# Kernel optimization log

Hardware: AMD Instinct MI355X
Metric: run time of the kernel (lower is better)

Reference implementation:

```python
import jax, jax.numpy as jnp
import numpy as np

IGNORE = -100000.0

def setup_inputs() -> dict:
    key = jax.random.key(0)
    ks = jax.random.split(key, 5)
    B, S, E, H, D = 4, 2048, 1024, 16, 64
    return {
        "x": jax.random.normal(ks[0], (B, S, E), dtype=jnp.float32),
        "W_Q": jax.random.normal(ks[1], (H, E, D), dtype=jnp.float32) * (E ** -0.5),
        "W_K": jax.random.normal(ks[2], (H, E, D), dtype=jnp.float32) * (E ** -0.5),
        "W_V": jax.random.normal(ks[3], (H, E, D), dtype=jnp.float32) * (E ** -0.5),
        "W_O": jax.random.normal(ks[4], (H, D, E), dtype=jnp.float32) * (D ** -0.5),
        "is_causal": 1,
    }

def reference(x, W_Q, W_K, W_V, W_O, is_causal):
    d_head = W_Q.shape[-1]
    # projections: [b, p, n_heads, d_head]
    q = jnp.einsum('nmd,bpm->bpnd', W_Q, x)
    k = jnp.einsum('nmd,bpm->bpnd', W_K, x)
    v = jnp.einsum('nmd,bpm->bpnd', W_V, x)
    # scores: [b, n_heads, q_pos, k_pos]
    scores = jnp.einsum('bqnd,bknd->bnqk', q, k) / np.sqrt(d_head).astype(jnp.float32)
    if is_causal:
        S = scores.shape[-1]
        mask = jnp.triu(jnp.ones((S, S), dtype=bool), k=1)  # True above diagonal
        scores = jnp.where(mask, jnp.float32(IGNORE), scores)
    attn = jax.nn.softmax(scores, axis=-1)
    # weighted values: [b, q_pos, n_heads, d_head]
    z = jnp.einsum('bknd,bnqk->bqnd', v, attn)
    # output projection: [b, q_pos, embed_dim]
    o = jnp.einsum('ndm,bqnd->bqm', W_O, z)
    # average_attn_weights=True -> mean over heads
    return o, attn.mean(axis=1)
```

## Files before the change

### kernel.cpp

```cpp
#include <hip/hip_runtime.h>
#include <stdint.h>


#define BB 4
#define SS 2048
#define EE 1024
#define HH 16
#define DD 64
#define MTOT (BB*SS)
#define HD (HH*DD)
#define QKV_ELEMS ((size_t)MTOT*HD)

typedef float f32x4 __attribute__((ext_vector_type(4)));
typedef short bf16x8 __attribute__((ext_vector_type(8)));

#define GLL(g, l) __builtin_amdgcn_global_load_lds( \
    (const __attribute__((address_space(1))) void*)(g), \
    (__attribute__((address_space(3))) void*)(l), 16, 0, 0)

__device__ __forceinline__ short f2bf(float f) {
    unsigned u = __builtin_bit_cast(unsigned, f);
    u += 0x7FFFu + ((u >> 16) & 1u);
    return (short)(u >> 16);
}

__global__ __launch_bounds__(256) void k_xcast(const float* __restrict__ x,
                                               short* __restrict__ xbf) {
    int i = blockIdx.x*256 + threadIdx.x;
    float4 f = ((const float4*)x)[i];
    short4 s; s.x=f2bf(f.x); s.y=f2bf(f.y); s.z=f2bf(f.z); s.w=f2bf(f.w);
    ((short4*)xbf)[i] = s;
}

__global__ __launch_bounds__(256) void k_wprep(const float* __restrict__ wq,
        const float* __restrict__ wk, const float* __restrict__ wv,
        const float* __restrict__ wo, short* __restrict__ wtq,
        short* __restrict__ wto) {
    __shared__ short Tl[64][72];
    int t = threadIdx.x, x = blockIdx.x, y = blockIdx.y;
    int r4 = t >> 2, c4 = (t & 3) << 4;
    if (y < 48) {
        int which = y >> 4, h = y & 15, e0 = x*64;
        const float* src = (which==0?wq:which==1?wk:wv) + (size_t)h*EE*DD;
        const float* p = src + (size_t)(e0 + r4)*DD + c4;
        #pragma unroll
        for (int j = 0; j < 4; ++j) {
            float4 f = ((const float4*)p)[j];
            Tl[r4][c4+j*4+0]=f2bf(f.x); Tl[r4][c4+j*4+1]=f2bf(f.y);
            Tl[r4][c4+j*4+2]=f2bf(f.z); Tl[r4][c4+j*4+3]=f2bf(f.w);
        }
        __syncthreads();
        size_t nrow = ((size_t)(which*16 + h))*64 + r4;
        #pragma unroll
        for (int i = 0; i < 16; ++i)
            wtq[nrow*1024 + e0 + c4 + i] = Tl[c4+i][r4];
    } else {
        int h = y - 48, e0 = x*64;
        const float* src = wo + (size_t)h*DD*EE;
        const float* p = src + (size_t)r4*EE + e0 + c4;
        #pragma unroll
        for (int j = 0; j < 4; ++j) {
            float4 f = ((const float4*)p)[j];
            Tl[r4][c4+j*4+0]=f2bf(f.x); Tl[r4][c4+j*4+1]=f2bf(f.y);
            Tl[r4][c4+j*4+2]=f2bf(f.z); Tl[r4][c4+j*4+3]=f2bf(f.w);
        }
        __syncthreads();
        #pragma unroll
        for (int i = 0; i < 16; ++i)
            wto[(size_t)(e0 + r4)*1024 + h*64 + c4 + i] = Tl[c4+i][r4];
    }
}

__global__ __launch_bounds__(256) void k_proj(const short* __restrict__ xbf,
        const short* __restrict__ wtq, short* __restrict__ qkv) {
    __shared__ short As[128*64];
    __shared__ short Bs[128*64];
    int t = threadIdx.x;
    int m0 = blockIdx.x*128, n0 = blockIdx.y*128;
    int lane = t & 63, l15 = lane & 15, quad = lane >> 4;
    int wm = (t>>6) >> 1, wn = (t>>6) & 1;
    f32x4 acc[4][4];
    #pragma unroll
    for (int i=0;i<4;++i)
        #pragma unroll
        for (int c=0;c<4;++c) acc[i][c] = (f32x4){0,0,0,0};

    for (int k0 = 0; k0 < EE; k0 += 64) {
        __syncthreads();
        #pragma unroll
        for (int j = 0; j < 4; ++j) {
            int c = j*256 + t;
            int row = c >> 3, cg = c & 7;
            GLL(xbf + (size_t)(m0+row)*EE + k0 + cg*8, &As[(j*256 + (t & 192))*8]);
            GLL(wtq + (size_t)(n0+row)*EE + k0 + cg*8, &Bs[(j*256 + (t & 192))*8]);
        }
        __syncthreads();
        #pragma unroll
        for (int kp = 0; kp < 64; kp += 32)
            #pragma unroll
            for (int i = 0; i < 4; ++i) {
                bf16x8 a = *(const bf16x8*)&As[(wm*64 + i*16 + l15)*64 + kp + quad*8];
                #pragma unroll
                for (int c = 0; c < 4; ++c) {
                    bf16x8 b = *(const bf16x8*)&Bs[(wn*64 + c*16 + l15)*64 + kp + quad*8];
                    acc[i][c] = __builtin_amdgcn_mfma_f32_16x16x32_bf16(a, b, acc[i][c], 0, 0, 0);
                }
            }
    }
    short* vt = qkv + 2*QKV_ELEMS;
    #pragma unroll
    for (int i = 0; i < 4; ++i)
        #pragma unroll
        for (int c = 0; c < 4; ++c) {
            int n = n0 + wn*64 + c*16 + l15;
            int row = m0 + wm*64 + i*16 + quad*4;
            if (n < 2048) {
                #pragma unroll
                for (int r = 0; r < 4; ++r)
                    qkv[(size_t)(n>>10)*QKV_ELEMS + (size_t)(row+r)*HD + (n & 1023)] =
                        f2bf(acc[i][c][r]);
            } else {
                short4 s4;
                s4.x = f2bf(acc[i][c][0]); s4.y = f2bf(acc[i][c][1]);
                s4.z = f2bf(acc[i][c][2]); s4.w = f2bf(acc[i][c][3]);
                int bb_ = row >> 11, pos = row & 2047;
                *(short4*)&vt[((size_t)bb_*HD + (n - 2048))*SS + pos] = s4;
            }
        }
}

__global__ __launch_bounds__(256) void k_attnz(const short* __restrict__ qws,
        const short* __restrict__ kws, const short* __restrict__ vtg,
        short* __restrict__ zws, float* __restrict__ c2ws) {
    __shared__ short Ks[64][72];
    __shared__ short Vt[64][72];
    __shared__ short Ps[4][32][72];
    int t = threadIdx.x;
    int h = blockIdx.y, b = blockIdx.z;
    int qx = (b & 1) ? (15 - blockIdx.x) : blockIdx.x;
    int q0 = qx*128;
    int w = t>>6, lane = t&63, l15 = lane&15, quad = lane>>4;
    int sr = t>>2, sc = (t&3)<<4;

    bf16x8 qr[2][2];
    #pragma unroll
    for (int mf=0; mf<2; ++mf)
        #pragma unroll
        for (int kp=0; kp<2; ++kp)
            qr[mf][kp] = *(const bf16x8*)(qws +
                (size_t)(b*SS + q0 + w*32 + mf*16 + l15)*HD + h*DD + kp*32 + quad*8);

    const short* ksrc = kws + (size_t)(b*SS + sr)*HD + h*DD + sc;
    const short* vsrc = vtg + ((size_t)b*HD + h*DD + sr)*SS + sc;

    f32x4 accz[2][4];
    f32x4 accl[2];
    #pragma unroll
    for (int mf=0;mf<2;++mf) {
        accl[mf] = (f32x4){0,0,0,0};
        #pragma unroll
        for (int c=0;c<4;++c) accz[mf][c] = (f32x4){0,0,0,0};
    }
    bf16x8 ones;
    #pragma unroll
    for (int i=0;i<8;++i) ones[i] = (short)0x3F80;
    const float SC = 0.125f * 1.4426950408889634f;
    int nk = q0/64 + 2;
    int qmax = q0 + w*32 + 31;

    uint4 pk0 = ((const uint4*)ksrc)[0], pk1 = ((const uint4*)ksrc)[1];
    uint4 pv0 = ((const uint4*)vsrc)[0], pv1 = ((const uint4*)vsrc)[1];

    for (int kt = 0; kt < nk; ++kt) {
        int k0 = kt*64;
        __syncthreads();
        *(uint4*)&Ks[sr][sc]   = pk0;  *(uint4*)&Ks[sr][sc+8] = pk1;
        *(uint4*)&Vt[sr][sc]   = pv0;  *(uint4*)&Vt[sr][sc+8] = pv1;
        __syncthreads();
        if (kt+1 < nk) {
            const uint4* kn = (const uint4*)(ksrc + (size_t)(k0+64)*HD);
            const uint4* vn = (const uint4*)(vsrc + (k0+64));
            pk0=kn[0]; pk1=kn[1]; pv0=vn[0]; pv1=vn[1];
        }
        if (k0 > qmax) continue;

        f32x4 s[2][4];
        #pragma unroll
        for (int mf=0;mf<2;++mf)
            #pragma unroll
            for (int c=0;c<4;++c) s[mf][c] = (f32x4){0,0,0,0};
        __builtin_amdgcn_s_setprio(1);
        #pragma unroll
        for (int c=0;c<4;++c)
            #pragma unroll
            for (int kp=0;kp<2;++kp) {
                bf16x8 bb = *(const bf16x8*)&Ks[c*16+l15][kp*32+quad*8];
                s[0][c] = __builtin_amdgcn_mfma_f32_16x16x32_bf16(qr[0][kp], bb, s[0][c], 0, 0, 0);
                s[1][c] = __builtin_amdgcn_mfma_f32_16x16x32_bf16(qr[1][kp], bb, s[1][c], 0, 0, 0);
            }
        __builtin_amdgcn_s_setprio(0);
        #pragma unroll
        for (int mf=0;mf<2;++mf) {
            int qg0 = q0 + w*32 + mf*16 + quad*4;
            #pragma unroll
            for (int c=0;c<4;++c) {
                int kg = k0 + c*16 + l15;
                #pragma unroll
                for (int r=0;r<4;++r) {
                    float p_ = (kg <= qg0+r) ? __builtin_amdgcn_exp2f(s[mf][c][r]*SC) : 0.0f;
                    Ps[w][mf*16 + quad*4 + r][c*16 + l15] = f2bf(p_);
                }
            }
        }
        __builtin_amdgcn_s_setprio(1);
        #pragma unroll
        for (int kp=0;kp<2;++kp) {
            bf16x8 pa0 = *(const bf16x8*)&Ps[w][l15][kp*32+quad*8];
            bf16x8 pa1 = *(const bf16x8*)&Ps[w][16+l15][kp*32+quad*8];
            #pragma unroll
            for (int cc=0;cc<4;++cc) {
                bf16x8 vb = *(const bf16x8*)&Vt[cc*16+l15][kp*32+quad*8];
                accz[0][cc] = __builtin_amdgcn_mfma_f32_16x16x32_bf16(pa0, vb, accz[0][cc], 0, 0, 0);
                accz[1][cc] = __builtin_amdgcn_mfma_f32_16x16x32_bf16(pa1, vb, accz[1][cc], 0, 0, 0);
            }
            accl[0] = __builtin_amdgcn_mfma_f32_16x16x32_bf16(pa0, ones, accl[0], 0, 0, 0);
            accl[1] = __builtin_amdgcn_mfma_f32_16x16x32_bf16(pa1, ones, accl[1], 0, 0, 0);
        }
        __builtin_amdgcn_s_setprio(0);
    }
    #pragma unroll
    for (int mf=0;mf<2;++mf) {
        float il[4];
        #pragma unroll
        for (int r=0;r<4;++r) il[r] = 1.0f / accl[mf][r];
        #pragma unroll
        for (int cc=0;cc<4;++cc)
            #pragma unroll
            for (int r=0;r<4;++r) {
                int row = q0 + w*32 + mf*16 + quad*4 + r;
                zws[(size_t)(b*SS+row)*HD + h*DD + cc*16 + l15] = f2bf(accz[mf][cc][r]*il[r]);
            }
        if (l15 == 0) {
            size_t base = ((size_t)(b*HH+h))*SS + q0 + w*32 + mf*16 + quad*4;
            #pragma unroll
            for (int r=0;r<4;++r)
                c2ws[base+r] = __log2f(accl[mf][r]);
        }
    }
}

__global__ __launch_bounds__(256) void k_mean(const short* __restrict__ qws,
        const short* __restrict__ kws, const float* __restrict__ c2ws,
        float* __restrict__ attn_out) {
    int b = blockIdx.z;
    int qx = (b & 1) ? (31 - (int)blockIdx.x) : (int)blockIdx.x;
    int q0 = qx*64, k0 = blockIdx.y*64;
    int t = threadIdx.x;
    if (k0 > q0) {
        int r = t >> 2, cq = (t & 3) << 4;
        float4 z4 = {0.f,0.f,0.f,0.f};
        float* dst = attn_out + ((size_t)(b*SS + q0 + r))*SS + k0 + cq;
        #pragma unroll
        for (int j = 0; j < 4; ++j) ((float4*)dst)[j] = z4;
        return;
    }
    __shared__ short Qs[2][64][72];
    __shared__ short Ks[2][64][72];
    __shared__ float c2s[16][64];
    int w = t>>6, lane = t&63, l15 = lane&15, quad = lane>>4;
    int sr = t>>2, sc = (t&3)<<4;
    #pragma unroll
    for (int i = 0; i < 4; ++i) {
        int idx = t + i*256;
        int h = idx >> 6, r = idx & 63;
        c2s[h][r] = c2ws[((size_t)(b*HH+h))*SS + q0 + r];
    }
    const short* qsrc = qws + (size_t)(b*SS + q0 + sr)*HD + sc;
    const short* ksrc = kws + (size_t)(b*SS + k0 + sr)*HD + sc;

    {
        const uint4* qp = (const uint4*)qsrc;
        const uint4* kp = (const uint4*)ksrc;
        uint4 a=qp[0], bq=qp[1], c=kp[0], d=kp[1];
        *(uint4*)&Qs[0][sr][sc]   = a;  *(uint4*)&Qs[0][sr][sc+8] = bq;
        *(uint4*)&Ks[0][sr][sc]   = c;  *(uint4*)&Ks[0][sr][sc+8] = d;
    }

    const float SC = 0.125f * 1.4426950408889634f;
    int rowg0 = q0 + w*16 + quad*4;
    f32x4 acc[4] = { {0,0,0,0},{0,0,0,0},{0,0,0,0},{0,0,0,0} };

    for (int h = 0; h < HH; ++h) {
        int cur = h & 1;
        __syncthreads();
        uint4 nqa, nqb, nka, nkb;
        if (h < HH-1) {
            const uint4* qn = (const uint4*)(qsrc + (h+1)*64);
            const uint4* kn = (const uint4*)(ksrc + (h+1)*64);
            nqa=qn[0]; nqb=qn[1]; nka=kn[0]; nkb=kn[1];
        }

        bf16x8 qa0 = *(const bf16x8*)&Qs[cur][w*16+l15][quad*8];
        bf16x8 qa1 = *(const bf16x8*)&Qs[cur][w*16+l15][quad*8+32];
        f32x4 c2 = *(const f32x4*)&c2s[h][w*16 + quad*4];
        #pragma unroll
        for (int ns = 0; ns < 4; ++ns) {
            bf16x8 b0 = *(const bf16x8*)&Ks[cur][ns*16+l15][quad*8];
            bf16x8 b1 = *(const bf16x8*)&Ks[cur][ns*16+l15][quad*8+32];
            f32x4 s = {0,0,0,0};
            s = __builtin_amdgcn_mfma_f32_16x16x32_bf16(qa0, b0, s, 0, 0, 0);
            s = __builtin_amdgcn_mfma_f32_16x16x32_bf16(qa1, b1, s, 0, 0, 0);
            int col = k0 + ns*16 + l15;
            #pragma unroll
            for (int r = 0; r < 4; ++r) {
                float ex = __builtin_amdgcn_exp2f(s[r]*SC - c2[r]);
                acc[ns][r] += (col <= rowg0 + r) ? ex : 0.0f;
            }
        }

        if (h < HH-1) {
            int nxt = cur ^ 1;
            *(uint4*)&Qs[nxt][sr][sc]   = nqa;  *(uint4*)&Qs[nxt][sr][sc+8] = nqb;
            *(uint4*)&Ks[nxt][sr][sc]   = nka;  *(uint4*)&Ks[nxt][sr][sc+8] = nkb;
        }
    }
    #pragma unroll
    for (int ns = 0; ns < 4; ++ns)
        #pragma unroll
        for (int r = 0; r < 4; ++r)
            attn_out[((size_t)(b*SS + rowg0 + r))*SS + k0 + ns*16 + l15] =
                acc[ns][r] * 0.0625f;
}

__global__ __launch_bounds__(256) void k_oproj(const short* __restrict__ zws,
        const short* __restrict__ wto, float* __restrict__ outp) {
    __shared__ short As[128*64];
    __shared__ short Bs[128*64];
    int t = threadIdx.x;
    int m0 = blockIdx.x*128, n0 = blockIdx.y*128;
    int lane = t & 63, l15 = lane & 15, quad = lane >> 4;
    int wm = (t>>6) >> 1, wn = (t>>6) & 1;
    f32x4 acc[4][4];
    #pragma unroll
    for (int i=0;i<4;++i)
        #pragma unroll
        for (int c=0;c<4;++c) acc[i][c] = (f32x4){0,0,0,0};

    for (int k0 = 0; k0 < HD; k0 += 64) {
        __syncthreads();
        #pragma unroll
        for (int j = 0; j < 4; ++j) {
            int c = j*256 + t;
            int row = c >> 3, cg = c & 7;
            GLL(zws + (size_t)(m0+row)*HD + k0 + cg*8, &As[(j*256 + (t & 192))*8]);
            GLL(wto + (size_t)(n0+row)*HD + k0 + cg*8, &Bs[(j*256 + (t & 192))*8]);
        }
        __syncthreads();
        #pragma unroll
        for (int kp = 0; kp < 64; kp += 32)
            #pragma unroll
            for (int i = 0; i < 4; ++i) {
                bf16x8 a = *(const bf16x8*)&As[(wm*64 + i*16 + l15)*64 + kp + quad*8];
                #pragma unroll
                for (int c = 0; c < 4; ++c) {
                    bf16x8 b = *(const bf16x8*)&Bs[(wn*64 + c*16 + l15)*64 + kp + quad*8];
                    acc[i][c] = __builtin_amdgcn_mfma_f32_16x16x32_bf16(a, b, acc[i][c], 0, 0, 0);
                }
            }
    }
    #pragma unroll
    for (int i = 0; i < 4; ++i)
        #pragma unroll
        for (int c = 0; c < 4; ++c)
            #pragma unroll
            for (int r = 0; r < 4; ++r) {
                int row = m0 + wm*64 + i*16 + quad*4 + r;
                int n = n0 + wn*64 + c*16 + l15;
                outp[(size_t)row*EE + n] = acc[i][c][r];
            }
}

extern "C" void kernel_launch(void* const* d_in, const int* in_sizes, int n_in,
                              void* d_out, int out_size, void* d_ws, size_t ws_size,
                              hipStream_t stream) {
    const float* x  = (const float*)d_in[0];
    const float* wq = (const float*)d_in[1];
    const float* wk = (const float*)d_in[2];
    const float* wv = (const float*)d_in[3];
    const float* wo = (const float*)d_in[4];

    short* xbf = (short*)d_ws;
    short* qb  = xbf + QKV_ELEMS;
    short* kb  = qb + QKV_ELEMS;
    short* vtb = kb + QKV_ELEMS;
    short* wtq = vtb + QKV_ELEMS;
    short* wto = wtq + (size_t)3*1024*1024;
    float* c2w = (float*)(wto + (size_t)1024*1024);
    short* zb  = xbf;

    float* o = (float*)d_out;
    float* attn_out = o + (size_t)MTOT*EE;

    k_xcast<<<dim3(8192),     256, 0, stream>>>(x, xbf);
    k_wprep<<<dim3(16,64),    256, 0, stream>>>(wq, wk, wv, wo, wtq, wto);
    k_proj <<<dim3(64,24),    256, 0, stream>>>(xbf, wtq, qb);
    k_attnz<<<dim3(16,16,4),  256, 0, stream>>>(qb, kb, vtb, zb, c2w);
    k_mean <<<dim3(32,32,4),  256, 0, stream>>>(qb, kb, c2w, attn_out);
    k_oproj<<<dim3(64,8),     256, 0, stream>>>(zb, wto, o);
}
```

Measured before the change: 391.0 us.

## Pair complementary causal query tiles per attention block and keep Q in registers

Each k_attnz block now processes two query tiles, qx and 15-qx, in one pass over the shared K/V stream. This balances causal work across blocks, halves the grid, and reuses each staged K/V tile for both. The QK^T MFMA operands are swapped so each lane holds consecutive keys, which lets P be written to LDS as short4 vectors. In k_mean, Q fragments are loaded straight from global memory into registers instead of being staged through double-buffered LDS, freeing LDS and some sync traffic at the cost of more registers.

Measured after the change: 402.0 us. +2.8%, slower.

```diff
diff --git a/kernel.cpp b/kernel.cpp
--- a/kernel.cpp
+++ b/kernel.cpp
@@ -137,39 +137,91 @@
     __shared__ short Ps[4][32][72];
     int t = threadIdx.x;
     int h = blockIdx.y, b = blockIdx.z;
-    int qx = (b & 1) ? (15 - blockIdx.x) : blockIdx.x;
-    int q0 = qx*128;
+    int bx = blockIdx.x;
+    int qxa = (b >= 2) ? (7 - bx) : bx;
+    int q0a = qxa*128, q0b = (15 - qxa)*128;
+    int nk  = 32 - 2*qxa;
     int w = t>>6, lane = t&63, l15 = lane&15, quad = lane>>4;
     int sr = t>>2, sc = (t&3)<<4;
 
-    bf16x8 qr[2][2];
-    #pragma unroll
-    for (int mf=0; mf<2; ++mf)
-        #pragma unroll
-        for (int kp=0; kp<2; ++kp)
-            qr[mf][kp] = *(const bf16x8*)(qws +
-                (size_t)(b*SS + q0 + w*32 + mf*16 + l15)*HD + h*DD + kp*32 + quad*8);
-
     const short* ksrc = kws + (size_t)(b*SS + sr)*HD + h*DD + sc;
     const short* vsrc = vtg + ((size_t)b*HD + h*DD + sr)*SS + sc;
 
-    f32x4 accz[2][4];
-    f32x4 accl[2];
+    bf16x8 qA[2][2], qB[2][2];
+    #pragma unroll
+    for (int mf=0; mf<2; ++mf)
+        #pragma unroll
+        for (int kp=0; kp<2; ++kp) {
+            qA[mf][kp] = *(const bf16x8*)(qws +
+                (size_t)(b*SS + q0a + w*32 + mf*16 + l15)*HD + h*DD + kp*32 + quad*8);
+            qB[mf][kp] = *(const bf16x8*)(qws +
+                (size_t)(b*SS + q0b + w*32 + mf*16 + l15)*HD + h*DD + kp*32 + quad*8);
+        }
+
+    f32x4 azA[2][4], azB[2][4], alA[2], alB[2];
     #pragma unroll
     for (int mf=0;mf<2;++mf) {
-        accl[mf] = (f32x4){0,0,0,0};
-        #pragma unroll
-        for (int c=0;c<4;++c) accz[mf][c] = (f32x4){0,0,0,0};
+        alA[mf] = (f32x4){0,0,0,0}; alB[mf] = (f32x4){0,0,0,0};
+        #pragma unroll
+        for (int c=0;c<4;++c) { azA[mf][c] = (f32x4){0,0,0,0}; azB[mf][c] = (f32x4){0,0,0,0}; }
     }
     bf16x8 ones;
     #pragma unroll
     for (int i=0;i<8;++i) ones[i] = (short)0x3F80;
     const float SC = 0.125f * 1.4426950408889634f;
-    int nk = q0/64 + 2;
-    int qmax = q0 + w*32 + 31;
+    int qmaxA = q0a + w*32 + 31, qmaxB = q0b + w*32 + 31;
 
     uint4 pk0 = ((const uint4*)ksrc)[0], pk1 = ((const uint4*)ksrc)[1];
     uint4 pv0 = ((const uint4*)vsrc)[0], pv1 = ((const uint4*)vsrc)[1];
+
+#define TILE(QF, AZ, AL, Q0, QMAX)                                             \
+    if (k0 <= (QMAX)) {                                                        \
+        f32x4 s_[2][4];                                                        \
+        _Pragma("unroll")                                                      \
+        for (int mf=0;mf<2;++mf)                                               \
+            _Pragma("unroll")                                                  \
+            for (int c=0;c<4;++c) s_[mf][c] = (f32x4){0,0,0,0};                \
+        __builtin_amdgcn_s_setprio(1);                                         \
+        _Pragma("unroll")                                                      \
+        for (int c=0;c<4;++c)                                                  \
+            _Pragma("unroll")                                                  \
+            for (int kp=0;kp<2;++kp) {                                         \
+                bf16x8 aK = *(const bf16x8*)&Ks[c*16+l15][kp*32+quad*8];       \
+                s_[0][c] = __builtin_amdgcn_mfma_f32_16x16x32_bf16(aK, QF[0][kp], s_[0][c], 0, 0, 0); \
+                s_[1][c] = __builtin_amdgcn_mfma_f32_16x16x32_bf16(aK, QF[1][kp], s_[1][c], 0, 0, 0); \
+            }                                                                  \
+        __builtin_amdgcn_s_setprio(0);                                         \
+        _Pragma("unroll")                                                      \
+        for (int mf=0;mf<2;++mf) {                                             \
+            int qg = (Q0) + w*32 + mf*16 + l15;                                \
+            _Pragma("unroll")                                                  \
+            for (int c=0;c<4;++c) {                                            \
+                int kb_ = k0 + c*16 + quad*4;                                  \
+                short4 s4;                                                     \
+                _Pragma("unroll")                                              \
+                for (int r=0;r<4;++r) {                                        \
+                    float p_ = (kb_ + r <= qg) ? __builtin_amdgcn_exp2f(s_[mf][c][r]*SC) : 0.0f; \
+                    ((short*)&s4)[r] = f2bf(p_);                               \
+                }                                                              \
+                *(short4*)&Ps[w][mf*16 + l15][c*16 + quad*4] = s4;             \
+            }                                                                  \
+        }                                                                      \
+        __builtin_amdgcn_s_setprio(1);                                         \
+        _Pragma("unroll")                                                      \
+        for (int kp=0;kp<2;++kp) {                                             \
+            bf16x8 pa0 = *(const bf16x8*)&Ps[w][l15][kp*32+quad*8];            \
+            bf16x8 pa1 = *(const bf16x8*)&Ps[w][16+l15][kp*32+quad*8];         \
+            _Pragma("unroll")                                                  \
+            for (int cc=0;cc<4;++cc) {                                         \
+                bf16x8 vb = *(const bf16x8*)&Vt[cc*16+l15][kp*32+quad*8];      \
+                AZ[0][cc] = __builtin_amdgcn_mfma_f32_16x16x32_bf16(pa0, vb, AZ[0][cc], 0, 0, 0); \
+                AZ[1][cc] = __builtin_amdgcn_mfma_f32_16x16x32_bf16(pa1, vb, AZ[1][cc], 0, 0, 0); \
+            }                                                                  \
+            AL[0] = __builtin_amdgcn_mfma_f32_16x16x32_bf16(pa0, ones, AL[0], 0, 0, 0); \
+            AL[1] = __builtin_amdgcn_mfma_f32_16x16x32_bf16(pa1, ones, AL[1], 0, 0, 0); \
+        }                                                                      \
+        __builtin_amdgcn_s_setprio(0);                                         \
+    }
 
     for (int kt = 0; kt < nk; ++kt) {
         int k0 = kt*64;
@@ -182,71 +234,35 @@
             const uint4* vn = (const uint4*)(vsrc + (k0+64));
             pk0=kn[0]; pk1=kn[1]; pv0=vn[0]; pv1=vn[1];
         }
-        if (k0 > qmax) continue;
-
-        f32x4 s[2][4];
-        #pragma unroll
-        for (int mf=0;mf<2;++mf)
-            #pragma unroll
-            for (int c=0;c<4;++c) s[mf][c] = (f32x4){0,0,0,0};
-        __builtin_amdgcn_s_setprio(1);
-        #pragma unroll
-        for (int c=0;c<4;++c)
-            #pragma unroll
-            for (int kp=0;kp<2;++kp) {
-                bf16x8 bb = *(const bf16x8*)&Ks[c*16+l15][kp*32+quad*8];
-                s[0][c] = __builtin_amdgcn_mfma_f32_16x16x32_bf16(qr[0][kp], bb, s[0][c], 0, 0, 0);
-                s[1][c] = __builtin_amdgcn_mfma_f32_16x16x32_bf16(qr[1][kp], bb, s[1][c], 0, 0, 0);
-            }
-        __builtin_amdgcn_s_setprio(0);
-        #pragma unroll
-        for (int mf=0;mf<2;++mf) {
-            int qg0 = q0 + w*32 + mf*16 + quad*4;
-            #pragma unroll
-            for (int c=0;c<4;++c) {
-                int kg = k0 + c*16 + l15;
-                #pragma unroll
-                for (int r=0;r<4;++r) {
-                    float p_ = (kg <= qg0+r) ? __builtin_amdgcn_exp2f(s[mf][c][r]*SC) : 0.0f;
-                    Ps[w][mf*16 + quad*4 + r][c*16 + l15] = f2bf(p_);
-                }
-            }
-        }
-        __builtin_amdgcn_s_setprio(1);
-        #pragma unroll
-        for (int kp=0;kp<2;++kp) {
-            bf16x8 pa0 = *(const bf16x8*)&Ps[w][l15][kp*32+quad*8];
-            bf16x8 pa1 = *(const bf16x8*)&Ps[w][16+l15][kp*32+quad*8];
-            #pragma unroll
-            for (int cc=0;cc<4;++cc) {
-                bf16x8 vb = *(const bf16x8*)&Vt[cc*16+l15][kp*32+quad*8];
-                accz[0][cc] = __builtin_amdgcn_mfma_f32_16x16x32_bf16(pa0, vb, accz[0][cc], 0, 0, 0);
-                accz[1][cc] = __builtin_amdgcn_mfma_f32_16x16x32_bf16(pa1, vb, accz[1][cc], 0, 0, 0);
-            }
-            accl[0] = __builtin_amdgcn_mfma_f32_16x16x32_bf16(pa0, ones, accl[0], 0, 0, 0);
-            accl[1] = __builtin_amdgcn_mfma_f32_16x16x32_bf16(pa1, ones, accl[1], 0, 0, 0);
-        }
-        __builtin_amdgcn_s_setprio(0);
-    }
-    #pragma unroll
-    for (int mf=0;mf<2;++mf) {
-        float il[4];
-        #pragma unroll
-        for (int r=0;r<4;++r) il[r] = 1.0f / accl[mf][r];
-        #pragma unroll
-        for (int cc=0;cc<4;++cc)
-            #pragma unroll
-            for (int r=0;r<4;++r) {
-                int row = q0 + w*32 + mf*16 + quad*4 + r;
-                zws[(size_t)(b*SS+row)*HD + h*DD + cc*16 + l15] = f2bf(accz[mf][cc][r]*il[r]);
-            }
-        if (l15 == 0) {
-            size_t base = ((size_t)(b*HH+h))*SS + q0 + w*32 + mf*16 + quad*4;
-            #pragma unroll
-            for (int r=0;r<4;++r)
-                c2ws[base+r] = __log2f(accl[mf][r]);
-        }
-    }
+        TILE(qB, azB, alB, q0b, qmaxB);
+        TILE(qA, azA, alA, q0a, qmaxA);
+    }
+#undef TILE
+
+#define EPI(AZ, AL, Q0)                                                        \
+    _Pragma("unroll")                                                          \
+    for (int mf=0;mf<2;++mf) {                                                 \
+        float il[4];                                                           \
+        _Pragma("unroll")                                                      \
+        for (int r=0;r<4;++r) il[r] = 1.0f / AL[mf][r];                        \
+        _Pragma("unroll")                                                      \
+        for (int cc=0;cc<4;++cc)                                               \
+            _Pragma("unroll")                                                  \
+            for (int r=0;r<4;++r) {                                            \
+                int row = (Q0) + w*32 + mf*16 + quad*4 + r;                    \
+                zws[(size_t)(b*SS+row)*HD + h*DD + cc*16 + l15] = f2bf(AZ[mf][cc][r]*il[r]); \
+            }                                                                  \
+        if (l15 == 0) {                                                        \
+            size_t base = ((size_t)(b*HH+h))*SS + (Q0) + w*32 + mf*16 + quad*4;\
+            _Pragma("unroll")                                                  \
+            for (int r=0;r<4;++r)                                              \
+                c2ws[base+r] = __log2f(AL[mf][r]);                             \
+        }                                                                      \
+    }
+
+    EPI(azB, alB, q0b);
+    EPI(azA, alA, q0a);
+#undef EPI
 }
 
 __global__ __launch_bounds__(256) void k_mean(const short* __restrict__ qws,
@@ -264,27 +280,26 @@
         for (int j = 0; j < 4; ++j) ((float4*)dst)[j] = z4;
         return;
     }
-    __shared__ short Qs[2][64][72];
-    __shared__ short Ks[2][64][72];
+    __shared__ short Ksm[2][64][72];
     __shared__ float c2s[16][64];
     int w = t>>6, lane = t&63, l15 = lane&15, quad = lane>>4;
     int sr = t>>2, sc = (t&3)<<4;
     #pragma unroll
     for (int i = 0; i < 4; ++i) {
         int idx = t + i*256;
-        int h = idx >> 6, r = idx & 63;
-        c2s[h][r] = c2ws[((size_t)(b*HH+h))*SS + q0 + r];
-    }
-    const short* qsrc = qws + (size_t)(b*SS + q0 + sr)*HD + sc;
+        int hh = idx >> 6, r = idx & 63;
+        c2s[hh][r] = c2ws[((size_t)(b*HH+hh))*SS + q0 + r];
+    }
     const short* ksrc = kws + (size_t)(b*SS + k0 + sr)*HD + sc;
+    const short* qsrc = qws + (size_t)(b*SS + q0 + w*16 + l15)*HD + quad*8;
 
     {
-        const uint4* qp = (const uint4*)qsrc;
         const uint4* kp = (const uint4*)ksrc;
-        uint4 a=qp[0], bq=qp[1], c=kp[0], d=kp[1];
-        *(uint4*)&Qs[0][sr][sc]   = a;  *(uint4*)&Qs[0][sr][sc+8] = bq;
-        *(uint4*)&Ks[0][sr][sc]   = c;  *(uint4*)&Ks[0][sr][sc+8] = d;
-    }
+        uint4 c = kp[0], d = kp[1];
+        *(uint4*)&Ksm[0][sr][sc] = c;  *(uint4*)&Ksm[0][sr][sc+8] = d;
+    }
+    bf16x8 qc0 = *(const bf16x8*)(qsrc);
+    bf16x8 qc1 = *(const bf16x8*)(qsrc + 32);
 
     const float SC = 0.125f * 1.4426950408889634f;
     int rowg0 = q0 + w*16 + quad*4;
@@ -293,23 +308,22 @@
     for (int h = 0; h < HH; ++h) {
         int cur = h & 1;
         __syncthreads();
-        uint4 nqa, nqb, nka, nkb;
+        uint4 nka, nkb; bf16x8 nq0, nq1;
         if (h < HH-1) {
-            const uint4* qn = (const uint4*)(qsrc + (h+1)*64);
             const uint4* kn = (const uint4*)(ksrc + (h+1)*64);
-            nqa=qn[0]; nqb=qn[1]; nka=kn[0]; nkb=kn[1];
-        }
-
-        bf16x8 qa0 = *(const bf16x8*)&Qs[cur][w*16+l15][quad*8];
-        bf16x8 qa1 = *(const bf16x8*)&Qs[cur][w*16+l15][quad*8+32];
+            nka = kn[0]; nkb = kn[1];
+            nq0 = *(const bf16x8*)(qsrc + (h+1)*64);
+            nq1 = *(const bf16x8*)(qsrc + (h+1)*64 + 32);
+        }
+
         f32x4 c2 = *(const f32x4*)&c2s[h][w*16 + quad*4];
         #pragma unroll
         for (int ns = 0; ns < 4; ++ns) {
-            bf16x8 b0 = *(const bf16x8*)&Ks[cur][ns*16+l15][quad*8];
-            bf16x8 b1 = *(const bf16x8*)&Ks[cur][ns*16+l15][quad*8+32];
+            bf16x8 b0 = *(const bf16x8*)&Ksm[cur][ns*16+l15][quad*8];
+            bf16x8 b1 = *(const bf16x8*)&Ksm[cur][ns*16+l15][quad*8+32];
             f32x4 s = {0,0,0,0};
-            s = __builtin_amdgcn_mfma_f32_16x16x32_bf16(qa0, b0, s, 0, 0, 0);
-            s = __builtin_amdgcn_mfma_f32_16x16x32_bf16(qa1, b1, s, 0, 0, 0);
+            s = __builtin_amdgcn_mfma_f32_16x16x32_bf16(qc0, b0, s, 0, 0, 0);
+            s = __builtin_amdgcn_mfma_f32_16x16x32_bf16(qc1, b1, s, 0, 0, 0);
             int col = k0 + ns*16 + l15;
             #pragma unroll
             for (int r = 0; r < 4; ++r) {
@@ -320,8 +334,8 @@
 
         if (h < HH-1) {
             int nxt = cur ^ 1;
-            *(uint4*)&Qs[nxt][sr][sc]   = nqa;  *(uint4*)&Qs[nxt][sr][sc+8] = nqb;
-            *(uint4*)&Ks[nxt][sr][sc]   = nka;  *(uint4*)&Ks[nxt][sr][sc+8] = nkb;
+            *(uint4*)&Ksm[nxt][sr][sc]   = nka;  *(uint4*)&Ksm[nxt][sr][sc+8] = nkb;
+            qc0 = nq0; qc1 = nq1;
         }
     }
     #pragma unroll
@@ -404,7 +418,7 @@
     k_xcast<<<dim3(8192),     256, 0, stream>>>(x, xbf);
     k_wprep<<<dim3(16,64),    256, 0, stream>>>(wq, wk, wv, wo, wtq, wto);
     k_proj <<<dim3(64,24),    256, 0, stream>>>(xbf, wtq, qb);
-    k_attnz<<<dim3(16,16,4),  256, 0, stream>>>(qb, kb, vtb, zb, c2w);
+    k_attnz<<<dim3(8,16,4),   256, 0, stream>>>(qb, kb, vtb, zb, c2w);
     k_mean <<<dim3(32,32,4),  256, 0, stream>>>(qb, kb, c2w, attn_out);
     k_oproj<<<dim3(64,8),     256, 0, stream>>>(zb, wto, o);
 }
```
